# Performance work log

Measured on AMD Instinct MI355X. Metric: run time of the kernel, lower is better.

Reference implementation:

```python
import jax, jax.numpy as jnp
import numpy as np

# Fixed Db4 filters (non-learnable buffers in the original module)
_H = np.array([-0.010597401785069032, 0.032883011666982945, 0.030841381835560764,
               -0.18703481171888114, -0.02798376941698385, 0.6308807679295904,
               0.7148465705529155, 0.2303778133088964], dtype=np.float32)
_G = np.array([(-1.0) ** k * v for k, v in enumerate(_H[::-1])], dtype=np.float32)

LEVELS = 5  # max(1, floor(log2(256)) - 3)


def _dwt_level(x, filt):
    """reflect-pad left (K-1), depthwise cross-correlation, stride-2 decimation.
    Equivalent to torch: F.pad(x,(K-1,0),'reflect') -> conv1d(groups=C) -> [..., ::2].
    Fused into a single strided conv since out[::2] == stride-2 conv from offset 0."""
    K = filt.shape[0]
    C = x.shape[1]
    xp = jnp.pad(x, ((0, 0), (0, 0), (K - 1, 0)), mode='reflect')
    w = jnp.broadcast_to(filt.reshape(1, 1, K), (C, 1, K))  # (C,1,K) depthwise
    return jax.lax.conv_general_dilated(
        xp, w, window_strides=(2,), padding='VALID',
        dimension_numbers=('NCH', 'OIH', 'NCH'), feature_group_count=C)


def _forward(x, db4_low, db4_high):
    approx = x
    details = []
    for _ in range(LEVELS):
        low = _dwt_level(approx, db4_low)
        high = _dwt_level(approx, db4_high)
        details.append(high)
        approx = low
    Fd = approx                    # final approximation  (B,C,S/32)
    Ft = details[-1]               # (B,C,S/32)
    Fa = details[-2]               # (B,C,S/16)
    Fb = details[-3]               # (B,C,S/8)
    Fg = details[-4]               # (B,C,S/4)
    FR = jnp.concatenate([Fd, Ft, Fa, Fb, Fg], axis=2)
    return (Fd, Ft, Fa, Fb, Fg, FR)


def setup_inputs() -> dict:
    key = jax.random.key(0)
    x = jax.random.normal(key, (64, 64, 16384), dtype=jnp.float32)
    return {"x": x, "db4_low": jnp.asarray(_H), "db4_high": jnp.asarray(_G)}


def reference(x, db4_low, db4_high):
    return _forward(x, db4_low, db4_high)
```

## Files before the change

kernel.cpp:

```cpp
#include <hip/hip_runtime.h>


static constexpr int SLEN = 16384;

typedef float f32x4 __attribute__((ext_vector_type(4)));

__device__ __forceinline__ int swz4(int f) {
    const int s = f >> 2;
    return (s ^ ((s >> 3) & 7)) << 2;
}
__device__ __forceinline__ int swz1(int f) {
    const int s = f >> 2;
    return (((s ^ ((s >> 3) & 7)) << 2) | (f & 3));
}

__device__ __forceinline__ float dotH(const float* w) {
    float s =      -0.010597401785069032f * w[0];
    s = fmaf( 0.032883011666982945f, w[1], s);
    s = fmaf( 0.030841381835560764f, w[2], s);
    s = fmaf(-0.18703481171888114f,  w[3], s);
    s = fmaf(-0.02798376941698385f,  w[4], s);
    s = fmaf( 0.6308807679295904f,   w[5], s);
    s = fmaf( 0.7148465705529155f,   w[6], s);
    s = fmaf( 0.2303778133088964f,   w[7], s);
    return s;
}
__device__ __forceinline__ float dotG(const float* w) {
    float s =       0.2303778133088964f * w[0];
    s = fmaf(-0.7148465705529155f,   w[1], s);
    s = fmaf( 0.6308807679295904f,   w[2], s);
    s = fmaf( 0.02798376941698385f,  w[3], s);
    s = fmaf(-0.18703481171888114f,  w[4], s);
    s = fmaf(-0.030841381835560764f, w[5], s);
    s = fmaf( 0.032883011666982945f, w[6], s);
    s = fmaf( 0.010597401785069032f, w[7], s);
    return s;
}

__device__ __forceinline__ void lw16s(const float* __restrict__ base, int foff, float* w) {
#pragma unroll
    for (int j = 0; j < 4; ++j) {
        const float4 v = *(const float4*)(base + swz4(foff + 4 * j));
        w[4*j+0] = v.x; w[4*j+1] = v.y; w[4*j+2] = v.z; w[4*j+3] = v.w;
    }
}
__device__ __forceinline__ void lw16s_q0(const float* __restrict__ base, float* w) {
#pragma unroll
    for (int i = 0; i < 16; ++i) { int m = i - 8; m = (m < 0) ? -m : m; w[i] = base[swz1(m)]; }
}

__device__ __forceinline__ void ntst4(float* p, float a0, float a1, float a2, float a3) {
    f32x4 v; v.x = a0; v.y = a1; v.z = a2; v.w = a3;
    __builtin_nontemporal_store(v, (f32x4*)p);
}

__device__ __forceinline__ void gl_lds16(const float* gp, float* lp) {
    __builtin_amdgcn_global_load_lds(
        (const __attribute__((address_space(1))) void*)gp,
        (__attribute__((address_space(3))) void*)lp, 16, 0, 0);
}

__device__ __forceinline__ void barrier_lds() {
    asm volatile("s_waitcnt lgkmcnt(0)" ::: "memory");
    __builtin_amdgcn_s_barrier();
    asm volatile("" ::: "memory");
}

__global__ __launch_bounds__(256, 6)
void dwt5_kernel(const float* __restrict__ x, float* __restrict__ out)
{
    __shared__ float buf[6528];
    const int bid = blockIdx.x;
    const int r   = bid >> 2;
    const int h   = bid & 3;
    const int tid = threadIdx.x;

    const float* __restrict__ xr = x + (size_t)r * SLEN;
    const size_t frBase = (size_t)33554432 + (size_t)r * 8192;

    const int X0  = h ? 4096*h - 256 : 0;
    const int A1s = h ? 2048*h - 120 : 0;
    const int A2s = h ? 1024*h - 56  : 0;
    const int A3s = h ?  512*h - 24  : 0;
    const int A4s = h ?  256*h - 8   : 0;
    constexpr int RA1 = 4352;
    constexpr int RA2 = 0;
    constexpr int RA3 = 2048;
    constexpr int RA4 = 3072;

    {
        const float* xsrc = xr + X0;
#pragma unroll
        for (int j = 0; j < 4; ++j) {
            const int L  = tid + 256*j;
            const int Ls = L ^ ((L >> 3) & 7);
            gl_lds16(xsrc + 4*Ls, buf + 4*L);
        }
        if (h != 0 && tid < 64) {
            const int L  = tid + 1024;
            const int Ls = L ^ ((L >> 3) & 7);
            gl_lds16(xsrc + 4*Ls, buf + 4*L);
        }
        asm volatile("s_waitcnt vmcnt(0)" ::: "memory");
    }
    barrier_lds();

    {
        const int g1lo = A1s >> 2;
        const int g1hi = 512 * (h + 1);
#pragma unroll
        for (int jj = 0; jj < 3; ++jj) {
            const int g = g1lo + tid + jj * 256;
            if (g < g1hi) {
                float w[16];
                if (g == 0) lw16s_q0(buf, w);
                else        lw16s(buf, 8 * g - 8 - X0, w);
                const float a0 = dotH(w + 1), a1 = dotH(w + 3), a2 = dotH(w + 5), a3 = dotH(w + 7);
                *(float4*)(buf + RA1 + swz4(4 * g - A1s)) = make_float4(a0, a1, a2, a3);
            }
        }
    }
    barrier_lds();

    {
        const int g2lo = A2s >> 2;
        const int g2hi = 256 * (h + 1);
        const int gd   = 256 * h;
        float* __restrict__ hi1 = out + (size_t)16777216 + (size_t)r * 4096;
        float* __restrict__ hi2 = out + frBase + 4096;
#pragma unroll
        for (int jj = 0; jj < 2; ++jj) {
            const int g = g2lo + tid + jj * 256;
            if (g < g2hi) {
                float w[16];
                if (g == 0) lw16s_q0(buf + RA1, w);
                else        lw16s(buf + RA1, 8 * g - 8 - A1s, w);
                const float a0 = dotH(w + 1), a1 = dotH(w + 3), a2 = dotH(w + 5), a3 = dotH(w + 7);
                *(float4*)(buf + RA2 + swz4(4 * g - A2s)) = make_float4(a0, a1, a2, a3);
                if (g >= gd) {
                    const float d0 = dotG(w + 1), d1 = dotG(w + 3), d2 = dotG(w + 5), d3 = dotG(w + 7);
                    ntst4(hi1 + 4 * g, d0, d1, d2, d3);
                    ntst4(hi2 + 4 * g, d0, d1, d2, d3);
                }
            }
        }
    }
    barrier_lds();

    {
        const int g3lo = A3s >> 2;
        const int g3hi = 128 * (h + 1);
        const int gd   = 128 * h;
        float* __restrict__ hi1 = out + (size_t)8388608 + (size_t)r * 2048;
        float* __restrict__ hi2 = out + frBase + 2048;
        const int g = g3lo + tid;
        if (g < g3hi) {
            float w[16];
            if (g == 0) lw16s_q0(buf + RA2, w);
            else        lw16s(buf + RA2, 8 * g - 8 - A2s, w);
            const float a0 = dotH(w + 1), a1 = dotH(w + 3), a2 = dotH(w + 5), a3 = dotH(w + 7);
            *(float4*)(buf + RA3 + swz4(4 * g - A3s)) = make_float4(a0, a1, a2, a3);
            if (g >= gd) {
                const float d0 = dotG(w + 1), d1 = dotG(w + 3), d2 = dotG(w + 5), d3 = dotG(w + 7);
                ntst4(hi1 + 4 * g, d0, d1, d2, d3);
                ntst4(hi2 + 4 * g, d0, d1, d2, d3);
            }
        }
    }
    barrier_lds();

    {
        const int g4lo = A4s >> 2;
        const int g4hi = 64 * (h + 1);
        const int gd   = 64 * h;
        float* __restrict__ hi1 = out + (size_t)4194304 + (size_t)r * 1024;
        float* __restrict__ hi2 = out + frBase + 1024;
        const int g = g4lo + tid;
        if (g < g4hi) {
            float w[16];
            if (g == 0) lw16s_q0(buf + RA3, w);
            else        lw16s(buf + RA3, 8 * g - 8 - A3s, w);
            const float a0 = dotH(w + 1), a1 = dotH(w + 3), a2 = dotH(w + 5), a3 = dotH(w + 7);
            *(float4*)(buf + RA4 + swz4(4 * g - A4s)) = make_float4(a0, a1, a2, a3);
            if (g >= gd) {
                const float d0 = dotG(w + 1), d1 = dotG(w + 3), d2 = dotG(w + 5), d3 = dotG(w + 7);
                ntst4(hi1 + 4 * g, d0, d1, d2, d3);
                ntst4(hi2 + 4 * g, d0, d1, d2, d3);
            }
        }
    }
    barrier_lds();

    if (tid < 32) {
        const int g = 32 * h + tid;
        float w[16];
        if (g == 0) lw16s_q0(buf + RA4, w);
        else        lw16s(buf + RA4, 8 * g - 8 - A4s, w);
        const float a0 = dotH(w + 1), a1 = dotH(w + 3), a2 = dotH(w + 5), a3 = dotH(w + 7);
        const float d0 = dotG(w + 1), d1 = dotG(w + 3), d2 = dotG(w + 5), d3 = dotG(w + 7);
        ntst4(out + (size_t)r * 512 + 4 * g,                   a0, a1, a2, a3);
        ntst4(out + frBase + 4 * g,                            a0, a1, a2, a3);
        ntst4(out + (size_t)2097152 + (size_t)r * 512 + 4 * g, d0, d1, d2, d3);
        ntst4(out + frBase + 512 + 4 * g,                      d0, d1, d2, d3);
    }
}

extern "C" void kernel_launch(void* const* d_in, const int* in_sizes, int n_in,
                              void* d_out, int out_size, void* d_ws, size_t ws_size,
                              hipStream_t stream) {
    const float* x = (const float*)d_in[0];
    float* out = (float*)d_out;
    dwt5_kernel<<<16384, 256, 0, stream>>>(x, out);
}
```

Before: 84.04 us.

## Load input in two chunks to shrink LDS and raise occupancy to 8 blocks

The input segment is staged into LDS in two halves instead of one, with level-1 computed in two passes, which cuts the shared buffer from 6528 to 4512 floats and relaxes launch bounds to 8 waves per SIMD. The aim is more resident blocks per CU to hide global load latency. The cost is an extra load phase and two extra barriers that serialize the load and compute of each half within a block.

```diff
diff --git a/kernel.cpp b/kernel.cpp
--- a/kernel.cpp
+++ b/kernel.cpp
@@ -66,10 +66,10 @@
     asm volatile("" ::: "memory");
 }
 
-__global__ __launch_bounds__(256, 6)
+__global__ __launch_bounds__(256, 8)
 void dwt5_kernel(const float* __restrict__ x, float* __restrict__ out)
 {
-    __shared__ float buf[6528];
+    __shared__ float buf[4512];
     const int bid = blockIdx.x;
     const int r   = bid >> 2;
     const int h   = bid & 3;
@@ -79,25 +79,30 @@
     const size_t frBase = (size_t)33554432 + (size_t)r * 8192;
 
     const int X0  = h ? 4096*h - 256 : 0;
+    const int XB  = X0 + 2016;
     const int A1s = h ? 2048*h - 120 : 0;
     const int A2s = h ? 1024*h - 56  : 0;
     const int A3s = h ?  512*h - 24  : 0;
     const int A4s = h ?  256*h - 8   : 0;
-    constexpr int RA1 = 4352;
+    constexpr int RA1 = 2336;
     constexpr int RA2 = 0;
-    constexpr int RA3 = 2048;
-    constexpr int RA4 = 3072;
+    constexpr int RA3 = 1088;
+    constexpr int RA4 = 1664;
+
+    const int g1lo = A1s >> 2;
+    const int g1hi = 512 * (h + 1);
+    const int gmid = g1lo + 256;
 
     {
         const float* xsrc = xr + X0;
 #pragma unroll
-        for (int j = 0; j < 4; ++j) {
+        for (int j = 0; j < 2; ++j) {
             const int L  = tid + 256*j;
             const int Ls = L ^ ((L >> 3) & 7);
             gl_lds16(xsrc + 4*Ls, buf + 4*L);
         }
-        if (h != 0 && tid < 64) {
-            const int L  = tid + 1024;
+        if (tid < 8) {
+            const int L  = 512 + tid;
             const int Ls = L ^ ((L >> 3) & 7);
             gl_lds16(xsrc + 4*Ls, buf + 4*L);
         }
@@ -106,15 +111,39 @@
     barrier_lds();
 
     {
-        const int g1lo = A1s >> 2;
-        const int g1hi = 512 * (h + 1);
-#pragma unroll
-        for (int jj = 0; jj < 3; ++jj) {
-            const int g = g1lo + tid + jj * 256;
+        const int g = g1lo + tid;
+        float w[16];
+        if (g == 0) lw16s_q0(buf, w);
+        else        lw16s(buf, 8 * g - 8 - X0, w);
+        const float a0 = dotH(w + 1), a1 = dotH(w + 3), a2 = dotH(w + 5), a3 = dotH(w + 7);
+        *(float4*)(buf + RA1 + swz4(4 * g - A1s)) = make_float4(a0, a1, a2, a3);
+    }
+    barrier_lds();
+
+    {
+        const float* xsrc = xr + XB;
+#pragma unroll
+        for (int j = 0; j < 2; ++j) {
+            const int L  = tid + 256*j;
+            const int Ls = L ^ ((L >> 3) & 7);
+            gl_lds16(xsrc + 4*Ls, buf + 4*L);
+        }
+        if (tid < 72) {
+            const int L  = 512 + tid;
+            const int Ls = L ^ ((L >> 3) & 7);
+            gl_lds16(xsrc + 4*Ls, buf + 4*L);
+        }
+        asm volatile("s_waitcnt vmcnt(0)" ::: "memory");
+    }
+    barrier_lds();
+
+    {
+#pragma unroll
+        for (int jj = 0; jj < 2; ++jj) {
+            const int g = gmid + tid + 256*jj;
             if (g < g1hi) {
                 float w[16];
-                if (g == 0) lw16s_q0(buf, w);
-                else        lw16s(buf, 8 * g - 8 - X0, w);
+                lw16s(buf, 8 * g - 8 - XB, w);
                 const float a0 = dotH(w + 1), a1 = dotH(w + 3), a2 = dotH(w + 5), a3 = dotH(w + 7);
                 *(float4*)(buf + RA1 + swz4(4 * g - A1s)) = make_float4(a0, a1, a2, a3);
             }
@@ -130,7 +159,7 @@
         float* __restrict__ hi2 = out + frBase + 4096;
 #pragma unroll
         for (int jj = 0; jj < 2; ++jj) {
-            const int g = g2lo + tid + jj * 256;
+            const int g = g2lo + tid + 256*jj;
             if (g < g2hi) {
                 float w[16];
                 if (g == 0) lw16s_q0(buf + RA1, w);
```

Result: no change. 85.24 us (+1.4%).
